# Optimization experiments

Measured on AMD Instinct MI355X. Metric: run time of the kernel, lower is better.

The kernel has to match this reference:

```python
import jax, jax.numpy as jnp
import numpy as np

N, B, S, A, H, E = 8, 8192, 64, 16, 512, 4  # agents, batch, state, action, hidden, heads
D = H // E  # attend_dim


def setup_inputs() -> dict:
    key = jax.random.key(0)
    ks = jax.random.split(key, 12)
    g = lambda k, shape, fan: (jax.random.normal(k, shape, jnp.float32) / np.float32(np.sqrt(fan)))
    return {
        "states": jax.random.normal(ks[0], (N, B, S), jnp.float32),
        "actions": jax.random.normal(ks[1], (N, B, A), jnp.float32),
        # per-agent state encoder (Linear + LeakyReLU)
        "Ws": g(ks[2], (N, S, H), S), "bs": jnp.zeros((N, H), jnp.float32),
        # per-agent state-action encoder
        "Wsa": g(ks[3], (N, S + A, H), S + A), "bsa": jnp.zeros((N, H), jnp.float32),
        # shared per-head extractors (key/selector bias-free, value has bias+LeakyReLU)
        "Wk": g(ks[4], (E, H, D), H),
        "Wsel": g(ks[5], (E, H, D), H),
        "Wv": g(ks[6], (E, H, D), H), "bv": jnp.zeros((E, D), jnp.float32),
        # per-agent critic head (2H -> H -> 1)
        "Wc1": g(ks[7], (N, 2 * H, H), 2 * H), "bc1": jnp.zeros((N, H), jnp.float32),
        "Wc2": g(ks[8], (N, H, 1), H), "bc2": jnp.zeros((N, 1), jnp.float32),
        # per-agent value head (2H -> H -> 1)
        "Wv1": g(ks[9], (N, 2 * H, H), 2 * H), "bv1": jnp.zeros((N, H), jnp.float32),
        "Wv2": g(ks[10], (N, H, 1), H), "bv2": jnp.zeros((N, 1), jnp.float32),
    }


def reference(states, actions, Ws, bs, Wsa, bsa, Wk, Wsel, Wv, bv,
              Wc1, bc1, Wc2, bc2, Wv1, bv1, Wv2, bv2):
    lrelu = jax.nn.leaky_relu  # slope 0.01, matches nn.LeakyReLU default
    # encoders: [N,B,H]
    s_enc = lrelu(jnp.einsum('nbs,nsh->nbh', states, Ws) + bs[:, None, :])
    sa = jnp.concatenate([states, actions], axis=-1)
    sa_enc = lrelu(jnp.einsum('nbi,nih->nbh', sa, Wsa) + bsa[:, None, :])
    # per-head keys/selectors/values: [B,E,N,D]
    keys = jnp.einsum('nbh,ehd->bend', sa_enc, Wk)
    sels = jnp.einsum('nbh,ehd->bend', sa_enc, Wsel)
    vals = lrelu(jnp.einsum('nbh,ehd->bend', sa_enc, Wv) + bv[None, :, None, :])
    # each agent i attends over all agents j (including itself; no mask in source)
    logits = jnp.einsum('beid,bejd->beij', sels, keys) / jnp.float32(np.sqrt(D))
    weights = jax.nn.softmax(logits, axis=-1)
    other = jnp.einsum('beij,bejd->beid', weights, vals)  # [B,E,N,D]
    other = jnp.transpose(other, (2, 0, 1, 3)).reshape(N, B, H)  # heads concat -> [N,B,H]
    critic_in = jnp.concatenate([sa_enc, other], axis=-1)  # [N,B,2H]
    value_in = jnp.concatenate([s_enc, other], axis=-1)
    q = jnp.einsum('nbh,nho->nbo', lrelu(jnp.einsum('nbi,nih->nbh', critic_in, Wc1) + bc1[:, None, :]), Wc2) + bc2[:, None, :]
    v = jnp.einsum('nbh,nho->nbo', lrelu(jnp.einsum('nbi,nih->nbh', value_in, Wv1) + bv1[:, None, :]), Wv2) + bv2[:, None, :]
    return q, v  # each [N,B,1]
```

## Files before the change

### kernel.cpp

```cpp
#include <hip/hip_runtime.h>


#define DEVI __device__ __forceinline__

typedef unsigned short us16;
typedef __bf16 bf16x8 __attribute__((ext_vector_type(8)));
typedef float f32x4 __attribute__((ext_vector_type(4)));
typedef unsigned short u16x8 __attribute__((ext_vector_type(8)));

DEVI us16 f2bf(float f) {
  unsigned u = __builtin_bit_cast(unsigned, f);
  u += 0x7FFFu + ((u >> 16) & 1u);
  return (us16)(u >> 16);
}
DEVI float bf2f(us16 h) {
  unsigned u = ((unsigned)h) << 16;
  return __builtin_bit_cast(float, u);
}
DEVI float lrelu(float v) { return v > 0.f ? v : 0.01f * v; }
DEVI int pk2(float a, float b) { return (int)f2bf(a) | ((int)f2bf(b) << 16); }

DEVI void gload16(const us16* g, us16* l) {
  __builtin_amdgcn_global_load_lds(
      (const __attribute__((address_space(1))) void*)g,
      (__attribute__((address_space(3))) void*)l, 16, 0, 0);
}

__global__ void tconv_k(const float* __restrict__ src, long srcSlice, int K, int O,
                        us16* __restrict__ dst, long dstSlice, int dstRowOff,
                        int ldd, int Kpad)
{
  __shared__ float t[32][33];
  const int s = blockIdx.z;
  const int k0 = blockIdx.x * 32, o0 = blockIdx.y * 32;
  const int lx = threadIdx.x, ly = threadIdx.y;
#pragma unroll
  for (int i = 0; i < 4; i++) {
    int k = k0 + ly + i * 8, o = o0 + lx;
    float v = 0.f;
    if (k < K && o < O) v = src[(long)s * srcSlice + (long)k * O + o];
    t[ly + i * 8][lx] = v;
  }
  __syncthreads();
#pragma unroll
  for (int i = 0; i < 4; i++) {
    int o = o0 + ly + i * 8, k = k0 + lx;
    if (o < O && k < Kpad)
      dst[(long)s * dstSlice + (long)(dstRowOff + o) * ldd + k] = f2bf(t[lx][ly + i * 8]);
  }
}

__global__ void tconv3_k(const float* __restrict__ wk, const float* __restrict__ wsel,
                         const float* __restrict__ wv, us16* __restrict__ dst)
{
  __shared__ float t[32][33];
  const int zz = blockIdx.z;
  const int e = zz & 3, m = zz >> 2;
  const float* src = ((m == 0) ? wk : (m == 1) ? wsel : wv) + (long)e * 512 * 128;
  us16* d = dst + (long)e * 384 * 512 + (long)(m * 128) * 512;
  const int k0 = blockIdx.x * 32, o0 = blockIdx.y * 32;
  const int lx = threadIdx.x, ly = threadIdx.y;
#pragma unroll
  for (int i = 0; i < 4; i++)
    t[ly + i * 8][lx] = src[(long)(k0 + ly + i * 8) * 128 + (o0 + lx)];
  __syncthreads();
#pragma unroll
  for (int i = 0; i < 4; i++)
    d[(long)(o0 + ly + i * 8) * 512 + (k0 + lx)] = f2bf(t[lx][ly + i * 8]);
}

__global__ void tconvC_k(const float* __restrict__ c1, const float* __restrict__ v1,
                         us16* __restrict__ dc, us16* __restrict__ dv)
{
  __shared__ float t[32][33];
  const int zz = blockIdx.z;
  const int n = zz & 7, m = zz >> 3;
  const float* src = ((m == 0) ? c1 : v1) + (long)n * 1024 * 512;
  us16* dst = ((m == 0) ? dc : dv) + (long)n * 512 * 1024;
  const int k0 = blockIdx.x * 32, o0 = blockIdx.y * 32;
  const int lx = threadIdx.x, ly = threadIdx.y;
#pragma unroll
  for (int i = 0; i < 4; i++)
    t[ly + i * 8][lx] = src[(long)(k0 + ly + i * 8) * 512 + (o0 + lx)];
  __syncthreads();
#pragma unroll
  for (int i = 0; i < 4; i++)
    dst[(long)(o0 + ly + i * 8) * 1024 + (k0 + lx)] = f2bf(t[lx][ly + i * 8]);
}

enum { ASRC_F32 = 2, ASRC_F32_CAT = 3 };

template <int ASRC, int KTOT>
__global__ __launch_bounds__(256, 4)
void enc_gemm_k(const float* __restrict__ Ap, long aSlice,
                const float* __restrict__ A2p, long a2Slice,
                const us16* __restrict__ Btp, long bSlice,
                const float* __restrict__ bias, long biasSlice,
                us16* __restrict__ outB, long outSlice, long outRow)
{
  __shared__ us16 lA[128 * 32];
  __shared__ us16 lB[128 * 32];
  const int tid = threadIdx.x;
  const int z = blockIdx.z;
  const int m0 = blockIdx.x * 128;
  const int n0 = blockIdx.y * 128;
  const int wv = tid >> 6, lane = tid & 63;
  const int wm = (wv >> 1) * 64, wn = (wv & 1) * 64;
  const int fr = lane & 15, fk = (lane >> 4) * 8;
  const int rbase = (lane >> 4) * 4;
  const int grow = tid >> 2, gcol = (tid & 3) * 8;

  f32x4 acc[4][4];
#pragma unroll
  for (int i = 0; i < 4; i++)
#pragma unroll
    for (int j = 0; j < 4; j++) acc[i][j] = f32x4{0.f, 0.f, 0.f, 0.f};

  const us16* bbase = Btp + (long)z * bSlice + (long)n0 * KTOT;

  for (int k0 = 0; k0 < KTOT; k0 += 32) {
    int4 ra0, ra1;
    {
      const int srow = tid >> 1, scol0 = (tid & 1) * 16;
      const int kg = k0 + scol0;
      const float* a = nullptr;
      if constexpr (ASRC == ASRC_F32) {
        a = Ap + (long)z * aSlice + (long)(m0 + srow) * 64 + kg;
      } else {
        if (kg < 64)      a = Ap + (long)z * aSlice + (long)(m0 + srow) * 64 + kg;
        else if (kg < 80) a = A2p + (long)z * a2Slice + (long)(m0 + srow) * 16 + (kg - 64);
      }
      float4 f0, f1, f2, f3;
      if (a) { const float4* ap = (const float4*)a; f0 = ap[0]; f1 = ap[1]; f2 = ap[2]; f3 = ap[3]; }
      else   { f0 = make_float4(0.f, 0.f, 0.f, 0.f); f1 = f0; f2 = f0; f3 = f0; }
      ra0.x = pk2(f0.x, f0.y); ra0.y = pk2(f0.z, f0.w); ra0.z = pk2(f1.x, f1.y); ra0.w = pk2(f1.z, f1.w);
      ra1.x = pk2(f2.x, f2.y); ra1.y = pk2(f2.z, f2.w); ra1.z = pk2(f3.x, f3.y); ra1.w = pk2(f3.z, f3.w);
    }

    __syncthreads();
    {
      const us16* bb = bbase + k0 + gcol;
      gload16(bb + (long)grow * KTOT, &lB[tid * 8]);
      gload16(bb + (long)(64 + grow) * KTOT, &lB[2048 + tid * 8]);
    }
    {
      const int srow = tid >> 1, scol0 = (tid & 1) * 16;
      *(int4*)&lA[srow * 32 + scol0]     = ra0;
      *(int4*)&lA[srow * 32 + scol0 + 8] = ra1;
    }
    __syncthreads();

    bf16x8 af[4], bfg[4];
#pragma unroll
    for (int f = 0; f < 4; f++) af[f]  = *(const bf16x8*)&lA[(wm + f * 16 + fr) * 32 + fk];
#pragma unroll
    for (int f = 0; f < 4; f++) bfg[f] = *(const bf16x8*)&lB[(wn + f * 16 + fr) * 32 + fk];
#pragma unroll
    for (int fm = 0; fm < 4; fm++)
#pragma unroll
      for (int fn = 0; fn < 4; fn++)
        acc[fm][fn] = __builtin_amdgcn_mfma_f32_16x16x32_bf16(af[fm], bfg[fn], acc[fm][fn], 0, 0, 0);
  }

#pragma unroll
  for (int fm = 0; fm < 4; fm++) {
#pragma unroll
    for (int fn = 0; fn < 4; fn++) {
      int col = n0 + wn + fn * 16 + fr;
      float badd = bias[(long)z * biasSlice + col];
      us16* op = outB + (long)z * outSlice + (long)(m0 + wm + fm * 16 + rbase) * outRow + col;
#pragma unroll
      for (int j = 0; j < 4; j++) {
        float v = lrelu(acc[fm][fn][j] + badd);
        op[(long)j * outRow] = f2bf(v);
      }
    }
  }
}

enum { EPI_KSV = 1, EPI_DOT = 2 };

template <bool CAT, int EPI, int KTOT>
__global__ __launch_bounds__(256, 4)
void gemm64_k(const us16* __restrict__ Ap, long aSlice,
              const us16* __restrict__ A2p, long a2Slice,
              const us16* __restrict__ Btp, long bSlice,
              const float* __restrict__ bias,
              us16* __restrict__ outB, long outSlice, long outRow,
              const float* __restrict__ dotW, float* __restrict__ partial)
{
  __shared__ us16 lA[128 * 64];
  __shared__ us16 lB[128 * 64];
  const int tid = threadIdx.x;
  const int z = blockIdx.z;
  const int m0 = blockIdx.x * 128;
  const int n0 = blockIdx.y * 128;
  const int wv = tid >> 6, lane = tid & 63;
  const int wm = (wv >> 1) * 64, wn = (wv & 1) * 64;
  const int fr = lane & 15, fk = (lane >> 4) * 8;
  const int rbase = (lane >> 4) * 4;
  const int xorkey = (fr & 7) << 3;

  f32x4 acc[4][4];
#pragma unroll
  for (int i = 0; i < 4; i++)
#pragma unroll
    for (int j = 0; j < 4; j++) acc[i][j] = f32x4{0.f, 0.f, 0.f, 0.f};

  const us16* bbase = Btp + (long)z * bSlice + (long)n0 * KTOT;

  for (int k0 = 0; k0 < KTOT; k0 += 64) {
    __syncthreads();
#pragma unroll
    for (int i = 0; i < 4; i++) {
      const int c = i * 256 + tid;
      const int r = c >> 3;
      const int col = ((c & 7) ^ (r & 7)) << 3;
      const us16* a;
      if constexpr (!CAT) {
        a = Ap + (long)z * aSlice + (long)(m0 + r) * KTOT + (k0 + col);
      } else {
        const int kg = k0 + col;
        a = (kg < 512) ? Ap  + (long)z * aSlice  + (long)(m0 + r) * 512 + kg
                       : A2p + (long)z * a2Slice + (long)(m0 + r) * 512 + (kg - 512);
      }
      gload16(a, &lA[c * 8]);
    }
#pragma unroll
    for (int i = 0; i < 4; i++) {
      const int c = i * 256 + tid;
      const int r = c >> 3;
      const int col = ((c & 7) ^ (r & 7)) << 3;
      gload16(bbase + (long)r * KTOT + (k0 + col), &lB[c * 8]);
    }
    __syncthreads();

#pragma unroll
    for (int ks = 0; ks < 2; ks++) {
      bf16x8 af[4], bfg[4];
      const int kc = ks * 32 + fk;
#pragma unroll
      for (int f = 0; f < 4; f++)
        af[f]  = *(const bf16x8*)&lA[(wm + f * 16 + fr) * 64 + (kc ^ xorkey)];
#pragma unroll
      for (int f = 0; f < 4; f++)
        bfg[f] = *(const bf16x8*)&lB[(wn + f * 16 + fr) * 64 + (kc ^ xorkey)];
#pragma unroll
      for (int fm = 0; fm < 4; fm++)
#pragma unroll
        for (int fn = 0; fn < 4; fn++)
          acc[fm][fn] = __builtin_amdgcn_mfma_f32_16x16x32_bf16(af[fm], bfg[fn], acc[fm][fn], 0, 0, 0);
    }
  }

  if constexpr (EPI == EPI_DOT) {
    const float* bsl = bias + (long)z * 512;
    const float* wsl = dotW + (long)z * 512;
#pragma unroll
    for (int fm = 0; fm < 4; fm++) {
#pragma unroll
      for (int j = 0; j < 4; j++) {
        float p = 0.f;
#pragma unroll
        for (int fn = 0; fn < 4; fn++) {
          int col = n0 + wn + fn * 16 + fr;
          float v = acc[fm][fn][j] + bsl[col];
          v = lrelu(v);
          p += v * wsl[col];
        }
        p += __shfl_xor(p, 1); p += __shfl_xor(p, 2); p += __shfl_xor(p, 4); p += __shfl_xor(p, 8);
        if (fr == 0) {
          long row = (long)z * 8192 + (m0 + wm + fm * 16 + rbase + j);
          partial[row * 8 + blockIdx.y * 2 + (wv & 1)] = p;
        }
      }
    }
  } else {
#pragma unroll
    for (int fm = 0; fm < 4; fm++) {
#pragma unroll
      for (int fn = 0; fn < 4; fn++) {
        int col = n0 + wn + fn * 16 + fr;
        float badd = 0.f; bool act = false;
        if (col >= 256) { badd = bias[col - 256]; act = true; }
        us16* op = outB + (long)z * outSlice + (long)(m0 + wm + fm * 16 + rbase) * outRow + col;
#pragma unroll
        for (int j = 0; j < 4; j++) {
          float v = acc[fm][fn][j] + badd;
          if (act) v = lrelu(v);
          op[(long)j * outRow] = f2bf(v);
        }
      }
    }
  }
}

template <bool CAT, int KTOT>
__global__ __launch_bounds__(512, 2)
void gemm256_k(const us16* __restrict__ Ap, long aSlice,
               const us16* __restrict__ A2p, long a2Slice,
               const us16* __restrict__ Btp, long bSlice,
               const float* __restrict__ bias,
               const float* __restrict__ dotW, float* __restrict__ partial)
{
  extern __shared__ us16 lds[];
  const int tid = threadIdx.x;
  const int z = blockIdx.z;
  const int m0 = blockIdx.x * 256;
  const int n0 = blockIdx.y * 256;
  const int wv = tid >> 6, lane = tid & 63;
  const int wr = wv >> 2, wc = wv & 3;
  const int wmBase = wr * 128, wnBase = wc * 64;
  const int fr = lane & 15, fk = (lane >> 4) * 8;
  const int rbase = (lane >> 4) * 4;

  const int srow = tid >> 3;
  const int scol = ((tid & 7) ^ (srow & 7)) << 3;

  f32x4 acc[8][4];
#pragma unroll
  for (int i = 0; i < 8; i++)
#pragma unroll
    for (int j = 0; j < 4; j++) acc[i][j] = f32x4{0.f, 0.f, 0.f, 0.f};

  const us16* bb = Btp + (long)z * bSlice + (long)n0 * KTOT;

  auto stA = [&](int dbuf, int k0, int g) {
    const int r = g * 64 + srow;
    const us16* a;
    if constexpr (CAT) {
      a = (k0 < 512) ? Ap  + (long)z * aSlice  + (long)(m0 + r) * 512 + (k0 + scol)
                     : A2p + (long)z * a2Slice + (long)(m0 + r) * 512 + (k0 - 512 + scol);
    } else {
      a = Ap + (long)z * aSlice + (long)(m0 + r) * KTOT + (k0 + scol);
    }
    gload16(a, lds + dbuf * 32768 + g * 4096 + tid * 8);
  };
  auto stB = [&](int dbuf, int k0, int g) {
    const int r = g * 64 + srow;
    gload16(bb + (long)r * KTOT + (k0 + scol), lds + dbuf * 32768 + 16384 + g * 4096 + tid * 8);
  };

  constexpr int NT = KTOT / 64;
#pragma unroll
  for (int g = 0; g < 4; g++) { stA(0, 0, g); stB(0, 0, g); }

#pragma unroll 1
  for (int t = 0; t < NT; ++t) {
    const int d = t & 1;
    const us16* curA = lds + d * 32768;
    const us16* curB = lds + d * 32768 + 16384;
    const int kn = (t + 1) * 64;
    const bool more = (t + 1 < NT);

    asm volatile("s_waitcnt vmcnt(0)" ::: "memory");
    __builtin_amdgcn_sched_barrier(0);
    __builtin_amdgcn_s_barrier();
    __builtin_amdgcn_sched_barrier(0);

    bf16x8 bfg[4][2];
#pragma unroll
    for (int fb = 0; fb < 4; fb++)
#pragma unroll
      for (int ks = 0; ks < 2; ks++) {
        const int row = wnBase + fb * 16 + fr;
        bfg[fb][ks] = *(const bf16x8*)&curB[row * 64 + ((ks * 32 + fk) ^ ((row & 7) << 3))];
      }

#pragma unroll
    for (int p = 0; p < 4; p++) {
      bf16x8 af[2][2];
#pragma unroll
      for (int f = 0; f < 2; f++)
#pragma unroll
        for (int ks = 0; ks < 2; ks++) {
          const int row = wmBase + (2 * p + f) * 16 + fr;
          af[f][ks] = *(const bf16x8*)&curA[row * 64 + ((ks * 32 + fk) ^ ((row & 7) << 3))];
        }
      if (more && p == 0) { stA(d ^ 1, kn, 0); stA(d ^ 1, kn, 1); stB(d ^ 1, kn, 0); stB(d ^ 1, kn, 1); }
      if (more && p == 1) { stA(d ^ 1, kn, 2); stA(d ^ 1, kn, 3); stB(d ^ 1, kn, 2); stB(d ^ 1, kn, 3); }
      __builtin_amdgcn_sched_barrier(0);
      __builtin_amdgcn_s_barrier();
      __builtin_amdgcn_s_setprio(1);
#pragma unroll
      for (int f = 0; f < 2; f++)
#pragma unroll
        for (int fn = 0; fn < 4; fn++)
#pragma unroll
          for (int ks = 0; ks < 2; ks++)
            acc[2 * p + f][fn] =
                __builtin_amdgcn_mfma_f32_16x16x32_bf16(af[f][ks], bfg[fn][ks], acc[2 * p + f][fn], 0, 0, 0);
      __builtin_amdgcn_s_setprio(0);
      __builtin_amdgcn_sched_barrier(0);
      __builtin_amdgcn_s_barrier();
      __builtin_amdgcn_sched_barrier(0);
    }
  }

  const float* bsl = bias + (long)z * 512;
  const float* wsl = dotW + (long)z * 512;
#pragma unroll
  for (int fm = 0; fm < 8; fm++) {
#pragma unroll
    for (int j = 0; j < 4; j++) {
      float p = 0.f;
#pragma unroll
      for (int fn = 0; fn < 4; fn++) {
        int col = n0 + wnBase + fn * 16 + fr;
        float v = acc[fm][fn][j] + bsl[col];
        v = lrelu(v);
        p += v * wsl[col];
      }
      p += __shfl_xor(p, 1); p += __shfl_xor(p, 2); p += __shfl_xor(p, 4); p += __shfl_xor(p, 8);
      if (fr == 0) {
        long row = (long)z * 8192 + (m0 + wmBase + fm * 16 + rbase + j);
        partial[row * 8 + blockIdx.y * 4 + wc] = p;
      }
    }
  }
}

__global__ __launch_bounds__(256, 4)
void attn_k(const us16* __restrict__ ksv, us16* __restrict__ other, int e)
{
  __shared__ us16 t[4][8 * 392];
  const int wv = threadIdx.x >> 6, lane = threadIdx.x & 63;
  const long b = (long)blockIdx.x * 4 + wv;
  const us16* src = ksv + b * 3072;
#pragma unroll
  for (int i = 0; i < 6; i++) {
    int c = i * 64 + lane;
    int r = c / 48, cc = c - r * 48;
    *(int4*)&t[wv][r * 392 + cc * 8] = *(const int4*)&src[c * 8];
  }
  __syncthreads();
  const int i = lane >> 3, j = lane & 7;
  const us16* selp = &t[wv][i * 392 + 128];
  const us16* keyp = &t[wv][j * 392];
  float acc = 0.f;
#pragma unroll
  for (int d = 0; d < 128; d += 8) {
    u16x8 s8 = *(const u16x8*)&selp[d];
    u16x8 k8 = *(const u16x8*)&keyp[d];
#pragma unroll
    for (int q = 0; q < 8; q++) acc += bf2f(s8[q]) * bf2f(k8[q]);
  }
  acc *= 0.088388347648318447f;
  float mx = acc;
  mx = fmaxf(mx, __shfl_xor(mx, 1)); mx = fmaxf(mx, __shfl_xor(mx, 2)); mx = fmaxf(mx, __shfl_xor(mx, 4));
  float ex = __expf(acc - mx);
  float sm = ex;
  sm += __shfl_xor(sm, 1); sm += __shfl_xor(sm, 2); sm += __shfl_xor(sm, 4);
  float wsm = ex / sm;
  float wj[8];
  const int ibase = lane & 56;
#pragma unroll
  for (int jj = 0; jj < 8; jj++) wj[jj] = __shfl(wsm, ibase + jj);
  const int dbase = (lane & 7) * 16;
  float o[16];
#pragma unroll
  for (int q = 0; q < 16; q++) o[q] = 0.f;
#pragma unroll
  for (int jj = 0; jj < 8; jj++) {
    u16x8 v0 = *(const u16x8*)&t[wv][jj * 392 + 256 + dbase];
    u16x8 v1 = *(const u16x8*)&t[wv][jj * 392 + 256 + dbase + 8];
    float wgt = wj[jj];
#pragma unroll
    for (int q = 0; q < 8; q++) { o[q] += wgt * bf2f(v0[q]); o[8 + q] += wgt * bf2f(v1[q]); }
  }
  u16x8 r0, r1;
#pragma unroll
  for (int q = 0; q < 8; q++) { r0[q] = f2bf(o[q]); r1[q] = f2bf(o[8 + q]); }
  us16* dst = other + ((long)i * 8192 + b) * 512 + e * 128 + dbase;
  *(u16x8*)&dst[0] = r0;
  *(u16x8*)&dst[8] = r1;
}

__global__ void reduce2_k(const float* __restrict__ part, const float* __restrict__ b2c,
                          const float* __restrict__ b2v, float* __restrict__ out)
{
  int r = blockIdx.x * 256 + threadIdx.x;
  const float4* p = (const float4*)(part + (long)r * 8);
  float4 a = p[0], b = p[1];
  float s = ((a.x + a.y) + (a.z + a.w)) + ((b.x + b.y) + (b.z + b.w));
  int agent = (r >> 13) & 7;
  out[r] = s + ((r < 65536) ? b2c[agent] : b2v[agent]);
}

extern "C" void kernel_launch(void* const* d_in, const int* in_sizes, int n_in,
                              void* d_out, int out_size, void* d_ws, size_t ws_size,
                              hipStream_t stream)
{
  const float* states = (const float*)d_in[0];
  const float* actions= (const float*)d_in[1];
  const float* Ws  = (const float*)d_in[2];
  const float* bs  = (const float*)d_in[3];
  const float* Wsa = (const float*)d_in[4];
  const float* bsa = (const float*)d_in[5];
  const float* Wk  = (const float*)d_in[6];
  const float* Wsel= (const float*)d_in[7];
  const float* Wv  = (const float*)d_in[8];
  const float* bv  = (const float*)d_in[9];
  const float* Wc1 = (const float*)d_in[10];
  const float* bc1 = (const float*)d_in[11];
  const float* Wc2 = (const float*)d_in[12];
  const float* bc2 = (const float*)d_in[13];
  const float* Wv1 = (const float*)d_in[14];
  const float* bv1 = (const float*)d_in[15];
  const float* Wv2 = (const float*)d_in[16];
  const float* bv2 = (const float*)d_in[17];

  char* ws = (char*)d_ws;
  constexpr size_t OFF_WST   = 0;
  constexpr size_t OFF_WSAT  = OFF_WST   + (size_t)8 * 512 * 64 * 2;
  constexpr size_t OFF_WKVST = OFF_WSAT  + (size_t)8 * 512 * 96 * 2;
  constexpr size_t OFF_WC1T  = OFF_WKVST + (size_t)4 * 384 * 512 * 2;
  constexpr size_t OFF_WV1T  = OFF_WC1T  + (size_t)8 * 512 * 1024 * 2;
  constexpr size_t OFF_ENC   = OFF_WV1T  + (size_t)8 * 512 * 1024 * 2;
  constexpr size_t OFF_OTHER = OFF_ENC   + (size_t)8 * 8192 * 512 * 2;
  constexpr size_t OFF_KSV   = OFF_OTHER + (size_t)8 * 8192 * 512 * 2;
  constexpr size_t OFF_PART  = OFF_KSV   + (size_t)8192 * 8 * 384 * 2;
  constexpr size_t NEED      = OFF_PART  + (size_t)131072 * 8 * 4;
  if (ws_size < NEED) return;

  us16* WST   = (us16*)(ws + OFF_WST);
  us16* WSAT  = (us16*)(ws + OFF_WSAT);
  us16* WKVST = (us16*)(ws + OFF_WKVST);
  us16* WC1T  = (us16*)(ws + OFF_WC1T);
  us16* WV1T  = (us16*)(ws + OFF_WV1T);
  us16* ENC   = (us16*)(ws + OFF_ENC);
  us16* OTHER = (us16*)(ws + OFF_OTHER);
  us16* KSV   = (us16*)(ws + OFF_KSV);
  float* PART = (float*)(ws + OFF_PART);

  const bool big =
      hipFuncSetAttribute((const void*)gemm256_k<true, 1024>,
                          hipFuncAttributeMaxDynamicSharedMemorySize, 131072) == hipSuccess;

  dim3 tb(32, 8);
  tconv_k <<<dim3(2, 16, 8),  tb, 0, stream>>>(Ws,  (long)64 * 512, 64, 512, WST,  (long)512 * 64, 0, 64, 64);
  tconv_k <<<dim3(3, 16, 8),  tb, 0, stream>>>(Wsa, (long)80 * 512, 80, 512, WSAT, (long)512 * 96, 0, 96, 96);
  tconv3_k<<<dim3(16, 4, 12), tb, 0, stream>>>(Wk, Wsel, Wv, WKVST);
  tconvC_k<<<dim3(32, 16, 16),tb, 0, stream>>>(Wc1, Wv1, WC1T, WV1T);

  enc_gemm_k<ASRC_F32_CAT, 96><<<dim3(64, 4, 8), 256, 0, stream>>>(
      states, (long)8192 * 64, actions, (long)8192 * 16, WSAT, (long)512 * 96, bsa, 512,
      ENC, (long)8192 * 512, 512);

  for (int e = 0; e < 4; e++) {
    gemm64_k<false, EPI_KSV, 512><<<dim3(64, 3, 8), 256, 0, stream>>>(
        ENC, (long)8192 * 512, nullptr, 0, WKVST + (size_t)e * 384 * 512, 0, bv + e * 128,
        KSV, 384, 3072, nullptr, nullptr);
    attn_k<<<dim3(2048), 256, 0, stream>>>(KSV, OTHER, e);
  }

  if (big) {
    gemm256_k<true, 1024><<<dim3(32, 2, 8), 512, 131072, stream>>>(
        ENC, (long)8192 * 512, OTHER, (long)8192 * 512, WC1T, (long)512 * 1024, bc1, Wc2, PART);
  } else {
    gemm64_k<true, EPI_DOT, 1024><<<dim3(64, 4, 8), 256, 0, stream>>>(
        ENC, (long)8192 * 512, OTHER, (long)8192 * 512, WC1T, (long)512 * 1024, bc1,
        nullptr, 0, 0, Wc2, PART);
  }

  enc_gemm_k<ASRC_F32, 64><<<dim3(64, 4, 8), 256, 0, stream>>>(
      states, (long)8192 * 64, nullptr, 0, WST, (long)512 * 64, bs, 512,
      ENC, (long)8192 * 512, 512);

  if (big) {
    gemm256_k<true, 1024><<<dim3(32, 2, 8), 512, 131072, stream>>>(
        ENC, (long)8192 * 512, OTHER, (long)8192 * 512, WV1T, (long)512 * 1024, bv1, Wv2,
        PART + (size_t)65536 * 8);
  } else {
    gemm64_k<true, EPI_DOT, 1024><<<dim3(64, 4, 8), 256, 0, stream>>>(
        ENC, (long)8192 * 512, OTHER, (long)8192 * 512, WV1T, (long)512 * 1024, bv1,
        nullptr, 0, 0, Wv2, PART + (size_t)65536 * 8);
  }

  reduce2_k<<<dim3(512), 256, 0, stream>>>(PART, bc2, bv2, (float*)d_out);
}
```

Baseline: 429.0 us.

## Batch all attention heads and fuse critic/value GEMMs into single launches

Replaces the per-head loop of key/selector/value GEMM plus attention launches with one GEMM covering all four heads into a larger KSV buffer, followed by a single attention launch over a 2D grid. Computes the state encoder into a separate buffer up front so the critic and value hidden-layer GEMMs with dot epilogue run as one launch with a doubled grid. Removes the 256x256 pipelined GEMM with large dynamic LDS in favour of a simpler 128x128 tile kernel without prefetch overlap, and merges two weight-transpose launches. The new path needs more workspace and falls back to the old per-head path when it is not available.

After: 417.7 us. -2.6%, faster.

```diff
diff --git a/kernel.cpp b/kernel.cpp
--- a/kernel.cpp
+++ b/kernel.cpp
@@ -26,27 +26,30 @@
       (__attribute__((address_space(3))) void*)l, 16, 0, 0);
 }
 
-__global__ void tconv_k(const float* __restrict__ src, long srcSlice, int K, int O,
-                        us16* __restrict__ dst, long dstSlice, int dstRowOff,
-                        int ldd, int Kpad)
+__global__ void tconvSA_k(const float* __restrict__ wsrc, const float* __restrict__ wsasrc,
+                          us16* __restrict__ wst, us16* __restrict__ wsat)
 {
   __shared__ float t[32][33];
-  const int s = blockIdx.z;
+  const int zz = blockIdx.z;
+  const int m = zz >> 3, s = zz & 7;
+  const int K = m ? 80 : 64, Kpad = m ? 96 : 64;
+  const float* src = m ? (wsasrc + (long)s * 80 * 512) : (wsrc + (long)s * 64 * 512);
+  us16* dst = m ? (wsat + (long)s * 512 * 96) : (wst + (long)s * 512 * 64);
   const int k0 = blockIdx.x * 32, o0 = blockIdx.y * 32;
   const int lx = threadIdx.x, ly = threadIdx.y;
 #pragma unroll
   for (int i = 0; i < 4; i++) {
     int k = k0 + ly + i * 8, o = o0 + lx;
     float v = 0.f;
-    if (k < K && o < O) v = src[(long)s * srcSlice + (long)k * O + o];
+    if (k < K) v = src[(long)k * 512 + o];
     t[ly + i * 8][lx] = v;
   }
   __syncthreads();
 #pragma unroll
   for (int i = 0; i < 4; i++) {
     int o = o0 + ly + i * 8, k = k0 + lx;
-    if (o < O && k < Kpad)
-      dst[(long)s * dstSlice + (long)(dstRowOff + o) * ldd + k] = f2bf(t[lx][ly + i * 8]);
+    if (k < Kpad)
+      dst[(long)o * Kpad + k] = f2bf(t[lx][ly + i * 8]);
   }
 }
 
@@ -295,148 +298,197 @@
   }
 }
 
-template <bool CAT, int KTOT>
-__global__ __launch_bounds__(512, 2)
-void gemm256_k(const us16* __restrict__ Ap, long aSlice,
-               const us16* __restrict__ A2p, long a2Slice,
-               const us16* __restrict__ Btp, long bSlice,
-               const float* __restrict__ bias,
-               const float* __restrict__ dotW, float* __restrict__ partial)
-{
-  extern __shared__ us16 lds[];
+__global__ __launch_bounds__(256, 4)
+void ksv4_k(const us16* __restrict__ enc, const us16* __restrict__ wkvst,
+            const float* __restrict__ bv, us16* __restrict__ ksv4)
+{
+  __shared__ us16 lA[128 * 64];
+  __shared__ us16 lB[128 * 64];
+  constexpr int KTOT = 512;
   const int tid = threadIdx.x;
   const int z = blockIdx.z;
-  const int m0 = blockIdx.x * 256;
-  const int n0 = blockIdx.y * 256;
+  const int e = blockIdx.y / 3;
+  const int n0 = (blockIdx.y % 3) * 128;
+  const int m0 = blockIdx.x * 128;
   const int wv = tid >> 6, lane = tid & 63;
-  const int wr = wv >> 2, wc = wv & 3;
-  const int wmBase = wr * 128, wnBase = wc * 64;
+  const int wm = (wv >> 1) * 64, wn = (wv & 1) * 64;
   const int fr = lane & 15, fk = (lane >> 4) * 8;
   const int rbase = (lane >> 4) * 4;
-
-  const int srow = tid >> 3;
-  const int scol = ((tid & 7) ^ (srow & 7)) << 3;
-
-  f32x4 acc[8][4];
-#pragma unroll
-  for (int i = 0; i < 8; i++)
+  const int xorkey = (fr & 7) << 3;
+
+  f32x4 acc[4][4];
+#pragma unroll
+  for (int i = 0; i < 4; i++)
 #pragma unroll
     for (int j = 0; j < 4; j++) acc[i][j] = f32x4{0.f, 0.f, 0.f, 0.f};
 
-  const us16* bb = Btp + (long)z * bSlice + (long)n0 * KTOT;
-
-  auto stA = [&](int dbuf, int k0, int g) {
-    const int r = g * 64 + srow;
-    const us16* a;
-    if constexpr (CAT) {
-      a = (k0 < 512) ? Ap  + (long)z * aSlice  + (long)(m0 + r) * 512 + (k0 + scol)
-                     : A2p + (long)z * a2Slice + (long)(m0 + r) * 512 + (k0 - 512 + scol);
-    } else {
-      a = Ap + (long)z * aSlice + (long)(m0 + r) * KTOT + (k0 + scol);
-    }
-    gload16(a, lds + dbuf * 32768 + g * 4096 + tid * 8);
-  };
-  auto stB = [&](int dbuf, int k0, int g) {
-    const int r = g * 64 + srow;
-    gload16(bb + (long)r * KTOT + (k0 + scol), lds + dbuf * 32768 + 16384 + g * 4096 + tid * 8);
-  };
-
-  constexpr int NT = KTOT / 64;
-#pragma unroll
-  for (int g = 0; g < 4; g++) { stA(0, 0, g); stB(0, 0, g); }
-
-#pragma unroll 1
-  for (int t = 0; t < NT; ++t) {
-    const int d = t & 1;
-    const us16* curA = lds + d * 32768;
-    const us16* curB = lds + d * 32768 + 16384;
-    const int kn = (t + 1) * 64;
-    const bool more = (t + 1 < NT);
-
-    asm volatile("s_waitcnt vmcnt(0)" ::: "memory");
-    __builtin_amdgcn_sched_barrier(0);
-    __builtin_amdgcn_s_barrier();
-    __builtin_amdgcn_sched_barrier(0);
-
-    bf16x8 bfg[4][2];
-#pragma unroll
-    for (int fb = 0; fb < 4; fb++)
-#pragma unroll
-      for (int ks = 0; ks < 2; ks++) {
-        const int row = wnBase + fb * 16 + fr;
-        bfg[fb][ks] = *(const bf16x8*)&curB[row * 64 + ((ks * 32 + fk) ^ ((row & 7) << 3))];
-      }
-
-#pragma unroll
-    for (int p = 0; p < 4; p++) {
-      bf16x8 af[2][2];
-#pragma unroll
-      for (int f = 0; f < 2; f++)
-#pragma unroll
-        for (int ks = 0; ks < 2; ks++) {
-          const int row = wmBase + (2 * p + f) * 16 + fr;
-          af[f][ks] = *(const bf16x8*)&curA[row * 64 + ((ks * 32 + fk) ^ ((row & 7) << 3))];
-        }
-      if (more && p == 0) { stA(d ^ 1, kn, 0); stA(d ^ 1, kn, 1); stB(d ^ 1, kn, 0); stB(d ^ 1, kn, 1); }
-      if (more && p == 1) { stA(d ^ 1, kn, 2); stA(d ^ 1, kn, 3); stB(d ^ 1, kn, 2); stB(d ^ 1, kn, 3); }
-      __builtin_amdgcn_sched_barrier(0);
-      __builtin_amdgcn_s_barrier();
-      __builtin_amdgcn_s_setprio(1);
-#pragma unroll
-      for (int f = 0; f < 2; f++)
+  const us16* abase = enc + (long)z * 8192 * 512 + (long)m0 * KTOT;
+  const us16* bbase = wkvst + ((long)e * 384 + n0) * KTOT;
+
+  for (int k0 = 0; k0 < KTOT; k0 += 64) {
+    __syncthreads();
+#pragma unroll
+    for (int i = 0; i < 4; i++) {
+      const int c = i * 256 + tid;
+      const int r = c >> 3;
+      const int col = ((c & 7) ^ (r & 7)) << 3;
+      gload16(abase + (long)r * KTOT + (k0 + col), &lA[c * 8]);
+    }
+#pragma unroll
+    for (int i = 0; i < 4; i++) {
+      const int c = i * 256 + tid;
+      const int r = c >> 3;
+      const int col = ((c & 7) ^ (r & 7)) << 3;
+      gload16(bbase + (long)r * KTOT + (k0 + col), &lB[c * 8]);
+    }
+    __syncthreads();
+
+#pragma unroll
+    for (int ks = 0; ks < 2; ks++) {
+      bf16x8 af[4], bfg[4];
+      const int kc = ks * 32 + fk;
+#pragma unroll
+      for (int f = 0; f < 4; f++)
+        af[f]  = *(const bf16x8*)&lA[(wm + f * 16 + fr) * 64 + (kc ^ xorkey)];
+#pragma unroll
+      for (int f = 0; f < 4; f++)
+        bfg[f] = *(const bf16x8*)&lB[(wn + f * 16 + fr) * 64 + (kc ^ xorkey)];
+#pragma unroll
+      for (int fm = 0; fm < 4; fm++)
 #pragma unroll
         for (int fn = 0; fn < 4; fn++)
-#pragma unroll
-          for (int ks = 0; ks < 2; ks++)
-            acc[2 * p + f][fn] =
-                __builtin_amdgcn_mfma_f32_16x16x32_bf16(af[f][ks], bfg[fn][ks], acc[2 * p + f][fn], 0, 0, 0);
-      __builtin_amdgcn_s_setprio(0);
-      __builtin_amdgcn_sched_barrier(0);
-      __builtin_amdgcn_s_barrier();
-      __builtin_amdgcn_sched_barrier(0);
+          acc[fm][fn] = __builtin_amdgcn_mfma_f32_16x16x32_bf16(af[fm], bfg[fn], acc[fm][fn], 0, 0, 0);
+    }
+  }
+
+#pragma unroll
+  for (int fm = 0; fm < 4; fm++) {
+#pragma unroll
+    for (int fn = 0; fn < 4; fn++) {
+      int col = n0 + wn + fn * 16 + fr;
+      float badd = 0.f; bool act = false;
+      if (col >= 256) { badd = bv[e * 128 + (col - 256)]; act = true; }
+      us16* op = ksv4 + (long)(m0 + wm + fm * 16 + rbase) * 12288 + e * 3072 + z * 384 + col;
+#pragma unroll
+      for (int j = 0; j < 4; j++) {
+        float v = acc[fm][fn][j] + badd;
+        if (act) v = lrelu(v);
+        op[(long)j * 12288] = f2bf(v);
+      }
+    }
+  }
+}
+
+__global__ __launch_bounds__(256, 4)
+void dot2_k(const us16* __restrict__ encC, const us16* __restrict__ encV,
+            const us16* __restrict__ other,
+            const us16* __restrict__ wc1t, const us16* __restrict__ wv1t,
+            const float* __restrict__ bc1, const float* __restrict__ bv1,
+            const float* __restrict__ wc2, const float* __restrict__ wv2,
+            float* __restrict__ partial)
+{
+  __shared__ us16 lA[128 * 64];
+  __shared__ us16 lB[128 * 64];
+  constexpr int KTOT = 1024;
+  const int tid = threadIdx.x;
+  const int zz = blockIdx.z;
+  const int half = zz >> 3, z = zz & 7;
+  const us16* Ap  = half ? encV : encC;
+  const us16* Btp = half ? wv1t : wc1t;
+  const float* bias = half ? bv1 : bc1;
+  const float* dotW = half ? wv2 : wc2;
+  const int m0 = blockIdx.x * 128;
+  const int n0 = blockIdx.y * 128;
+  const int wv = tid >> 6, lane = tid & 63;
+  const int wm = (wv >> 1) * 64, wn = (wv & 1) * 64;
+  const int fr = lane & 15, fk = (lane >> 4) * 8;
+  const int rbase = (lane >> 4) * 4;
+  const int xorkey = (fr & 7) << 3;
+
+  f32x4 acc[4][4];
+#pragma unroll
+  for (int i = 0; i < 4; i++)
+#pragma unroll
+    for (int j = 0; j < 4; j++) acc[i][j] = f32x4{0.f, 0.f, 0.f, 0.f};
+
+  const us16* bbase = Btp + (long)z * 512 * 1024 + (long)n0 * KTOT;
+  const long aSlice = (long)8192 * 512;
+
+  for (int k0 = 0; k0 < KTOT; k0 += 64) {
+    __syncthreads();
+#pragma unroll
+    for (int i = 0; i < 4; i++) {
+      const int c = i * 256 + tid;
+      const int r = c >> 3;
+      const int col = ((c & 7) ^ (r & 7)) << 3;
+      const int kg = k0 + col;
+      const us16* a = (kg < 512) ? Ap    + (long)z * aSlice + (long)(m0 + r) * 512 + kg
+                                 : other + (long)z * aSlice + (long)(m0 + r) * 512 + (kg - 512);
+      gload16(a, &lA[c * 8]);
+    }
+#pragma unroll
+    for (int i = 0; i < 4; i++) {
+      const int c = i * 256 + tid;
+      const int r = c >> 3;
+      const int col = ((c & 7) ^ (r & 7)) << 3;
+      gload16(bbase + (long)r * KTOT + (k0 + col), &lB[c * 8]);
+    }
+    __syncthreads();
+
+#pragma unroll
+    for (int ks = 0; ks < 2; ks++) {
+      bf16x8 af[4], bfg[4];
+      const int kc = ks * 32 + fk;
+#pragma unroll
+      for (int f = 0; f < 4; f++)
+        af[f]  = *(const bf16x8*)&lA[(wm + f * 16 + fr) * 64 + (kc ^ xorkey)];
+#pragma unroll
+      for (int f = 0; f < 4; f++)
+        bfg[f] = *(const bf16x8*)&lB[(wn + f * 16 + fr) * 64 + (kc ^ xorkey)];
+#pragma unroll
+      for (int fm = 0; fm < 4; fm++)
+#pragma unroll
+        for (int fn = 0; fn < 4; fn++)
+          acc[fm][fn] = __builtin_amdgcn_mfma_f32_16x16x32_bf16(af[fm], bfg[fn], acc[fm][fn], 0, 0, 0);
     }
   }
 
   const float* bsl = bias + (long)z * 512;
   const float* wsl = dotW + (long)z * 512;
 #pragma unroll
-  for (int fm = 0; fm < 8; fm++) {
+  for (int fm = 0; fm < 4; fm++) {
 #pragma unroll
     for (int j = 0; j < 4; j++) {
       float p = 0.f;
 #pragma unroll
       for (int fn = 0; fn < 4; fn++) {
-        int col = n0 + wnBase + fn * 16 + fr;
+        int col = n0 + wn + fn * 16 + fr;
         float v = acc[fm][fn][j] + bsl[col];
         v = lrelu(v);
         p += v * wsl[col];
       }
       p += __shfl_xor(p, 1); p += __shfl_xor(p, 2); p += __shfl_xor(p, 4); p += __shfl_xor(p, 8);
       if (fr == 0) {
-        long row = (long)z * 8192 + (m0 + wmBase + fm * 16 + rbase + j);
-        partial[row * 8 + blockIdx.y * 4 + wc] = p;
-      }
-    }
-  }
-}
-
-__global__ __launch_bounds__(256, 4)
-void attn_k(const us16* __restrict__ ksv, us16* __restrict__ other, int e)
-{
-  __shared__ us16 t[4][8 * 392];
-  const int wv = threadIdx.x >> 6, lane = threadIdx.x & 63;
-  const long b = (long)blockIdx.x * 4 + wv;
-  const us16* src = ksv + b * 3072;
+        long row = (long)half * 65536 + (long)z * 8192 + (m0 + wm + fm * 16 + rbase + j);
+        partial[row * 8 + blockIdx.y * 2 + (wv & 1)] = p;
+      }
+    }
+  }
+}
+
+DEVI void attn_core(const us16* __restrict__ src, us16* __restrict__ other,
+                    int e, long b, int wv, int lane, us16* tbuf)
+{
 #pragma unroll
   for (int i = 0; i < 6; i++) {
     int c = i * 64 + lane;
     int r = c / 48, cc = c - r * 48;
-    *(int4*)&t[wv][r * 392 + cc * 8] = *(const int4*)&src[c * 8];
+    *(int4*)&tbuf[r * 392 + cc * 8] = *(const int4*)&src[c * 8];
   }
   __syncthreads();
   const int i = lane >> 3, j = lane & 7;
-  const us16* selp = &t[wv][i * 392 + 128];
-  const us16* keyp = &t[wv][j * 392];
+  const us16* selp = &tbuf[i * 392 + 128];
+  const us16* keyp = &tbuf[j * 392];
   float acc = 0.f;
 #pragma unroll
   for (int d = 0; d < 128; d += 8) {
@@ -462,8 +514,8 @@
   for (int q = 0; q < 16; q++) o[q] = 0.f;
 #pragma unroll
   for (int jj = 0; jj < 8; jj++) {
-    u16x8 v0 = *(const u16x8*)&t[wv][jj * 392 + 256 + dbase];
-    u16x8 v1 = *(const u16x8*)&t[wv][jj * 392 + 256 + dbase + 8];
+    u16x8 v0 = *(const u16x8*)&tbuf[jj * 392 + 256 + dbase];
+    u16x8 v1 = *(const u16x8*)&tbuf[jj * 392 + 256 + dbase + 8];
     float wgt = wj[jj];
 #pragma unroll
     for (int q = 0; q < 8; q++) { o[q] += wgt * bf2f(v0[q]); o[8 + q] += wgt * bf2f(v1[q]); }
@@ -474,6 +526,25 @@
   us16* dst = other + ((long)i * 8192 + b) * 512 + e * 128 + dbase;
   *(u16x8*)&dst[0] = r0;
   *(u16x8*)&dst[8] = r1;
+}
+
+__global__ __launch_bounds__(256, 4)
+void attn_k(const us16* __restrict__ ksv, us16* __restrict__ other, int e)
+{
+  __shared__ us16 t[4][8 * 392];
+  const int wv = threadIdx.x >> 6, lane = threadIdx.x & 63;
+  const long b = (long)blockIdx.x * 4 + wv;
+  attn_core(ksv + b * 3072, other, e, b, wv, lane, &t[wv][0]);
+}
+
+__global__ __launch_bounds__(256, 4)
+void attn4_k(const us16* __restrict__ ksv4, us16* __restrict__ other)
+{
+  __shared__ us16 t[4][8 * 392];
+  const int wv = threadIdx.x >> 6, lane = threadIdx.x & 63;
+  const long b = (long)blockIdx.x * 4 + wv;
+  const int e = blockIdx.y;
+  attn_core(ksv4 + b * 12288 + e * 3072, other, e, b, wv, lane, &t[wv][0]);
 }
 
 __global__ void reduce2_k(const float* __restrict__ part, const float* __restrict__ b2c,
@@ -519,9 +590,13 @@
   constexpr size_t OFF_ENC   = OFF_WV1T  + (size_t)8 * 512 * 1024 * 2;
   constexpr size_t OFF_OTHER = OFF_ENC   + (size_t)8 * 8192 * 512 * 2;
   constexpr size_t OFF_KSV   = OFF_OTHER + (size_t)8 * 8192 * 512 * 2;
-  constexpr size_t OFF_PART  = OFF_KSV   + (size_t)8192 * 8 * 384 * 2;
-  constexpr size_t NEED      = OFF_PART  + (size_t)131072 * 8 * 4;
-  if (ws_size < NEED) return;
+  constexpr size_t OFF_PARTB = OFF_KSV   + (size_t)8192 * 8 * 384 * 2;
+  constexpr size_t NEED_B    = OFF_PARTB + (size_t)131072 * 8 * 4;
+  constexpr size_t OFF_PARTA = OFF_KSV   + (size_t)65536 * 1536 * 2;
+  constexpr size_t OFF_ENC2  = OFF_PARTA + (size_t)131072 * 8 * 4;
+  constexpr size_t NEED_A    = OFF_ENC2  + (size_t)8 * 8192 * 512 * 2;
+  if (ws_size < NEED_B) return;
+  const bool bigws = (ws_size >= NEED_A);
 
   us16* WST   = (us16*)(ws + OFF_WST);
   us16* WSAT  = (us16*)(ws + OFF_WSAT);
@@ -531,51 +606,44 @@
   us16* ENC   = (us16*)(ws + OFF_ENC);
   us16* OTHER = (us16*)(ws + OFF_OTHER);
   us16* KSV   = (us16*)(ws + OFF_KSV);
-  float* PART = (float*)(ws + OFF_PART);
-
-  const bool big =
-      hipFuncSetAttribute((const void*)gemm256_k<true, 1024>,
-                          hipFuncAttributeMaxDynamicSharedMemorySize, 131072) == hipSuccess;
+  float* PARTB= (float*)(ws + OFF_PARTB);
+  float* PARTA= (float*)(ws + OFF_PARTA);
+  us16* ENC2  = (us16*)(ws + OFF_ENC2);
 
   dim3 tb(32, 8);
-  tconv_k <<<dim3(2, 16, 8),  tb, 0, stream>>>(Ws,  (long)64 * 512, 64, 512, WST,  (long)512 * 64, 0, 64, 64);
-  tconv_k <<<dim3(3, 16, 8),  tb, 0, stream>>>(Wsa, (long)80 * 512, 80, 512, WSAT, (long)512 * 96, 0, 96, 96);
-  tconv3_k<<<dim3(16, 4, 12), tb, 0, stream>>>(Wk, Wsel, Wv, WKVST);
-  tconvC_k<<<dim3(32, 16, 16),tb, 0, stream>>>(Wc1, Wv1, WC1T, WV1T);
+  tconvSA_k<<<dim3(3, 16, 16), tb, 0, stream>>>(Ws, Wsa, WST, WSAT);
+  tconv3_k <<<dim3(16, 4, 12), tb, 0, stream>>>(Wk, Wsel, Wv, WKVST);
+  tconvC_k <<<dim3(32, 16, 16),tb, 0, stream>>>(Wc1, Wv1, WC1T, WV1T);
 
   enc_gemm_k<ASRC_F32_CAT, 96><<<dim3(64, 4, 8), 256, 0, stream>>>(
       states, (long)8192 * 64, actions, (long)8192 * 16, WSAT, (long)512 * 96, bsa, 512,
       ENC, (long)8192 * 512, 512);
 
-  for (int e = 0; e < 4; e++) {
-    gemm64_k<false, EPI_KSV, 512><<<dim3(64, 3, 8), 256, 0, stream>>>(
-        ENC, (long)8192 * 512, nullptr, 0, WKVST + (size_t)e * 384 * 512, 0, bv + e * 128,
-        KSV, 384, 3072, nullptr, nullptr);
-    attn_k<<<dim3(2048), 256, 0, stream>>>(KSV, OTHER, e);
-  }
-
-  if (big) {
-    gemm256_k<true, 1024><<<dim3(32, 2, 8), 512, 131072, stream>>>(
-        ENC, (long)8192 * 512, OTHER, (long)8192 * 512, WC1T, (long)512 * 1024, bc1, Wc2, PART);
+  if (bigws) {
+    enc_gemm_k<ASRC_F32, 64><<<dim3(64, 4, 8), 256, 0, stream>>>(
+        states, (long)8192 * 64, nullptr, 0, WST, (long)512 * 64, bs, 512,
+        ENC2, (long)8192 * 512, 512);
+    ksv4_k<<<dim3(64, 12, 8), 256, 0, stream>>>(ENC, WKVST, bv, KSV);
+    attn4_k<<<dim3(2048, 4), 256, 0, stream>>>(KSV, OTHER);
+    dot2_k<<<dim3(64, 4, 16), 256, 0, stream>>>(
+        ENC, ENC2, OTHER, WC1T, WV1T, bc1, bv1, Wc2, Wv2, PARTA);
+    reduce2_k<<<dim3(512), 256, 0, stream>>>(PARTA, bc2, bv2, (float*)d_out);
   } else {
+    for (int e = 0; e < 4; e++) {
+      gemm64_k<false, EPI_KSV, 512><<<dim3(64, 3, 8), 256, 0, stream>>>(
+          ENC, (long)8192 * 512, nullptr, 0, WKVST + (size_t)e * 384 * 512, 0, bv + e * 128,
+          KSV, 384, 3072, nullptr, nullptr);
+      attn_k<<<dim3(2048), 256, 0, stream>>>(KSV, OTHER, e);
+    }
     gemm64_k<true, EPI_DOT, 1024><<<dim3(64, 4, 8), 256, 0, stream>>>(
         ENC, (long)8192 * 512, OTHER, (long)8192 * 512, WC1T, (long)512 * 1024, bc1,
-        nullptr, 0, 0, Wc2, PART);
-  }
-
-  enc_gemm_k<ASRC_F32, 64><<<dim3(64, 4, 8), 256, 0, stream>>>(
-      states, (long)8192 * 64, nullptr, 0, WST, (long)512 * 64, bs, 512,
-      ENC, (long)8192 * 512, 512);
-
-  if (big) {
-    gemm256_k<true, 1024><<<dim3(32, 2, 8), 512, 131072, stream>>>(
-        ENC, (long)8192 * 512, OTHER, (long)8192 * 512, WV1T, (long)512 * 1024, bv1, Wv2,
-        PART + (size_t)65536 * 8);
-  } else {
+        nullptr, 0, 0, Wc2, PARTB);
+    enc_gemm_k<ASRC_F32, 64><<<dim3(64, 4, 8), 256, 0, stream>>>(
+        states, (long)8192 * 64, nullptr, 0, WST, (long)512 * 64, bs, 512,
+        ENC, (long)8192 * 512, 512);
     gemm64_k<true, EPI_DOT, 1024><<<dim3(64, 4, 8), 256, 0, stream>>>(
         ENC, (long)8192 * 512, OTHER, (long)8192 * 512, WV1T, (long)512 * 1024, bv1,
-        nullptr, 0, 0, Wv2, PART + (size_t)65536 * 8);
-  }
-
-  reduce2_k<<<dim3(512), 256, 0, stream>>>(PART, bc2, bv2, (float*)d_out);
-}
+        nullptr, 0, 0, Wv2, PARTB + (size_t)65536 * 8);
+    reduce2_k<<<dim3(512), 256, 0, stream>>>(PARTB, bc2, bv2, (float*)d_out);
+  }
+}
```
